# Optimization experiments

Hardware: AMD Instinct MI355X
Metric: run time of the kernel (lower is better)

Reference implementation:

```python
import jax, jax.numpy as jnp
import numpy as np

EPS = 1e-6
BASE_CURVATURE = 1.0


def _artanh(x):
    return jnp.arctanh(jnp.clip(x, -1.0 + 1e-5, 1.0 - 1e-5))


def _norm(x):
    return jnp.maximum(jnp.linalg.norm(x, axis=-1, keepdims=True), EPS)


def _logmap0(x, c):
    # Poincare-ball log map at origin
    sc = jnp.sqrt(c)
    n = _norm(x)
    return _artanh(sc * n) * x / (sc * n)


def _expmap0(v, c):
    # Poincare-ball exp map at origin
    sc = jnp.sqrt(c)
    n = _norm(v)
    return jnp.tanh(sc * n) * v / (sc * n)


def _mobius_add(x, y, c):
    x2 = jnp.sum(x * x, axis=-1, keepdims=True)
    y2 = jnp.sum(y * y, axis=-1, keepdims=True)
    xy = jnp.sum(x * y, axis=-1, keepdims=True)
    num = (1.0 + 2.0 * c * xy + c * y2) * x + (1.0 - c * x2) * y
    den = 1.0 + 2.0 * c * xy + (c * c) * x2 * y2
    return num / jnp.maximum(den, EPS)


def _mobius_scalar_mul(t, x, c):
    sc = jnp.sqrt(c)
    n = _norm(x)
    return jnp.tanh(t * _artanh(sc * n)) * x / (sc * n)


def setup_inputs() -> dict:
    key = jax.random.key(0)
    ks = jax.random.split(key, 8)
    B, D_in, D_out, K = 4096, 2048, 2048, 4
    scale_w = np.sqrt(2.0 / (D_in + D_out)) * 0.1
    return {
        "x": jax.random.normal(ks[0], (B, D_in), jnp.float32) * 0.05,
        "weight": jax.random.normal(ks[1], (D_out, D_in), jnp.float32) * scale_w,
        "bias": jax.random.normal(ks[2], (D_out,), jnp.float32) * 0.01,
        "curv_weight": jax.random.normal(ks[3], (1, D_in), jnp.float32) * 0.1,
        "curv_bias": jnp.zeros((1,), jnp.float32),
        "anchors": jax.random.normal(ks[4], (K, D_out), jnp.float32) * 0.3,
        "t_values": jnp.full((K,), 0.5, jnp.float32),
        "anchor_weights": jnp.full((K,), 1.0 / K, jnp.float32),
    }


def reference(x, weight, bias, curv_weight, curv_bias, anchors, t_values, anchor_weights):
    # 1) dynamic curvature prediction: c_i = base_c * softplus(x . w + b), then mean
    logits = x @ curv_weight[0] + curv_bias[0]                 # [B]
    curvatures = BASE_CURVATURE * jax.nn.softplus(logits)      # [B]
    c = jax.lax.stop_gradient(jnp.mean(curvatures))            # scalar (.item() in torch)

    # 2) fused hyperbolic linear: expmap0(logmap0(x) @ W^T + b)
    u = _logmap0(x, c)                                         # [B, D_in]
    h = u @ weight.T + bias                                    # [B, D_out]
    y = _expmap0(h, c)                                         # [B, D_out]

    # 3) geodesic activation: weighted Mobius geodesic toward each anchor
    xe = y[:, None, :]                                         # [B, 1, D]
    a = anchors[None, :, :]                                    # [1, K, D]
    diff = _mobius_add(-xe, a, c)                              # [B, K, D]
    step = _mobius_scalar_mul(t_values[None, :, None], diff, c)
    g = _mobius_add(xe, step, c)                               # [B, K, D]
    w = jax.nn.softmax(anchor_weights)                         # [K]
    return jnp.einsum("bkd,k->bd", g, w)                       # [B, D_out]
```

## Files before the change

kernel.cpp:

```cpp
#include <hip/hip_runtime.h>
#include <stdint.h>

#define B_ROWS 4096
#define D_IN   2048
#define D_OUT  2048
#define KANCH  4

typedef _Float16 half8  __attribute__((ext_vector_type(8)));
typedef _Float16 half4  __attribute__((ext_vector_type(4)));
typedef float    floatx4 __attribute__((ext_vector_type(4)));
typedef const __attribute__((address_space(1))) uint8_t* gptr_t;
typedef __attribute__((address_space(3))) uint8_t* lptr_t;

__device__ __forceinline__ float frcp(float x)   { return __builtin_amdgcn_rcpf(x); }
__device__ __forceinline__ float ftanh(float x)  { float e = __expf(2.f * x); return (e - 1.f) * frcp(e + 1.f); }
__device__ __forceinline__ float fatanh(float z) { return 0.5f * __logf((1.f + z) * frcp(1.f - z)); }

__global__ __launch_bounds__(256) void k_prep(
    const float* __restrict__ x,
    const float* __restrict__ W,
    const float* __restrict__ cw,
    const float* __restrict__ cb,
    const float* __restrict__ bias,
    const float* __restrict__ anchors,
    _Float16* __restrict__ xh,
    _Float16* __restrict__ Wh,
    float* __restrict__ n2x,
    float* __restrict__ spart,
    float* __restrict__ scal)
{
    int tid = threadIdx.x;
    if (blockIdx.x < 1024) {
        int w = tid >> 6, lane = tid & 63;
        int row = blockIdx.x * 4 + w;
        const floatx4* xr = (const floatx4*)(x + (size_t)row * D_IN);
        const floatx4* wr = (const floatx4*)cw;
        _Float16* xo = xh + (size_t)row * D_IN;
        float dot = 0.f, ss = 0.f;
#pragma unroll
        for (int i = 0; i < 8; ++i) {
            int idx = i * 64 + lane;
            floatx4 xv = xr[idx];
            floatx4 wv = wr[idx];
#pragma unroll
            for (int j = 0; j < 4; ++j) {
                dot += xv[j] * wv[j];
                ss  += xv[j] * xv[j];
            }
            half4 h = {(_Float16)xv[0], (_Float16)xv[1], (_Float16)xv[2], (_Float16)xv[3]};
            *(half4*)(xo + idx * 4) = h;
        }
#pragma unroll
        for (int off = 32; off; off >>= 1) {
            dot += __shfl_down(dot, off);
            ss  += __shfl_down(ss, off);
        }
        __shared__ float spw[4];
        if (lane == 0) {
            n2x[row] = ss;
            float z = dot + cb[0];
            spw[w] = (z > 20.f) ? z : log1pf(expf(z));
        }
        __syncthreads();
        if (tid == 0)
            spart[blockIdx.x] = spw[0] + spw[1] + spw[2] + spw[3];
    } else if (blockIdx.x < 2048) {
        int blk = blockIdx.x - 1024;
        const floatx4* W4 = (const floatx4*)W;
#pragma unroll
        for (int i = 0; i < 4; ++i) {
            int idx = blk * 1024 + i * 256 + tid;
            floatx4 v = W4[idx];
            half4 h = {(_Float16)v[0], (_Float16)v[1], (_Float16)v[2], (_Float16)v[3]};
            *(half4*)(Wh + (size_t)idx * 4) = h;
        }
    } else {
        int w = tid >> 6, lane = tid & 63;
        float bf[8], af[KANCH][8];
        *(floatx4*)(bf)     = *(const floatx4*)(bias + tid * 8);
        *(floatx4*)(bf + 4) = *(const floatx4*)(bias + tid * 8 + 4);
#pragma unroll
        for (int k = 0; k < KANCH; ++k) {
            *(floatx4*)(af[k])     = *(const floatx4*)(anchors + (size_t)k * D_OUT + tid * 8);
            *(floatx4*)(af[k] + 4) = *(const floatx4*)(anchors + (size_t)k * D_OUT + tid * 8 + 4);
        }
        float v[9];
#pragma unroll
        for (int q = 0; q < 9; ++q) v[q] = 0.f;
#pragma unroll
        for (int j = 0; j < 8; ++j) {
            v[0] += bf[j] * bf[j];
#pragma unroll
            for (int k = 0; k < KANCH; ++k) {
                v[1 + k] += bf[j] * af[k][j];
                v[5 + k] += af[k][j] * af[k][j];
            }
        }
#pragma unroll
        for (int off = 32; off; off >>= 1)
#pragma unroll
            for (int q = 0; q < 9; ++q) v[q] += __shfl_down(v[q], off);
        __shared__ float red[4][9];
        if (lane == 0)
#pragma unroll
            for (int q = 0; q < 9; ++q) red[w][q] = v[q];
        __syncthreads();
        if (tid == 0)
#pragma unroll
            for (int q = 0; q < 9; ++q)
                scal[1 + q] = red[0][q] + red[1][q] + red[2][q] + red[3][q];
    }
}

template<int KPB>
__global__ __launch_bounds__(256, 4) void k_gemm(
    const _Float16* __restrict__ A,
    const _Float16* __restrict__ W,
    _Float16* __restrict__ P0,
    _Float16* __restrict__ P1)
{
    __shared__ __align__(16) _Float16 As[128 * 64];
    __shared__ __align__(16) _Float16 Bs[128 * 64];
    int tid = threadIdx.x;
    int lane = tid & 63;
    int w = tid >> 6;
    int wm = (w >> 1) * 64, wn = (w & 1) * 64;
    int bm0 = blockIdx.y * 128, bn0 = blockIdx.x * 128;
    _Float16* P = (blockIdx.z == 0) ? P0 : P1;
    int kbase = blockIdx.z * KPB;

    floatx4 acc[4][4];
#pragma unroll
    for (int mi = 0; mi < 4; ++mi)
#pragma unroll
        for (int ni = 0; ni < 4; ++ni)
            acc[mi][ni] = (floatx4){0.f, 0.f, 0.f, 0.f};

    for (int k0 = 0; k0 < KPB; k0 += 64) {
#pragma unroll
        for (int i = 0; i < 4; ++i) {
            int e = (i * 256 + tid) * 8;
            int r = e >> 6, kk = e & 63;
            __builtin_amdgcn_global_load_lds(
                (gptr_t)(A + (size_t)(bm0 + r) * D_IN + kbase + k0 + kk),
                (lptr_t)(As + e), 16, 0, 0);
            __builtin_amdgcn_global_load_lds(
                (gptr_t)(W + (size_t)(bn0 + r) * D_IN + kbase + k0 + kk),
                (lptr_t)(Bs + e), 16, 0, 0);
        }
        __syncthreads();
#pragma unroll
        for (int ks = 0; ks < 64; ks += 32) {
            int kq = ks + (lane >> 4) * 8;
            half8 afr[4], bfr[4];
#pragma unroll
            for (int mi = 0; mi < 4; ++mi)
                afr[mi] = *(const half8*)(As + (wm + mi * 16 + (lane & 15)) * 64 + kq);
#pragma unroll
            for (int ni = 0; ni < 4; ++ni)
                bfr[ni] = *(const half8*)(Bs + (wn + ni * 16 + (lane & 15)) * 64 + kq);
#pragma unroll
            for (int mi = 0; mi < 4; ++mi)
#pragma unroll
                for (int ni = 0; ni < 4; ++ni)
                    acc[mi][ni] = __builtin_amdgcn_mfma_f32_16x16x32_f16(
                        afr[mi], bfr[ni], acc[mi][ni], 0, 0, 0);
        }
        __syncthreads();
    }
#pragma unroll
    for (int mi = 0; mi < 4; ++mi) {
#pragma unroll
        for (int r = 0; r < 4; ++r) {
            int gm = bm0 + wm + mi * 16 + (lane >> 4) * 4 + r;
#pragma unroll
            for (int ni = 0; ni < 4; ++ni) {
                int gn = bn0 + wn + ni * 16 + (lane & 15);
                P[(size_t)gm * D_OUT + gn] = (_Float16)acc[mi][ni][r];
            }
        }
    }
}

__global__ __launch_bounds__(256) void k_mobius(
    const _Float16* __restrict__ P0,
    const _Float16* __restrict__ P1,
    const float* __restrict__ bias,
    const float* __restrict__ anchors,
    const float* __restrict__ tv,
    const float* __restrict__ aw,
    const float* __restrict__ n2x,
    const float* __restrict__ spart,
    const float* __restrict__ scal,
    int split,
    float* __restrict__ out)
{
    int tid = threadIdx.x, w = tid >> 6, lane = tid & 63;
    size_t rowoff = (size_t)blockIdx.x * D_OUT;
    float pf[8], bf[8];
    {
        half8 p = *(const half8*)(P0 + rowoff + tid * 8);
#pragma unroll
        for (int j = 0; j < 8; ++j) pf[j] = (float)p[j];
    }
    if (split == 2) {
        half8 q = *(const half8*)(P1 + rowoff + tid * 8);
#pragma unroll
        for (int j = 0; j < 8; ++j) pf[j] += (float)q[j];
    }
    *(floatx4*)(bf)     = *(const floatx4*)(bias + tid * 8);
    *(floatx4*)(bf + 4) = *(const floatx4*)(bias + tid * 8 + 4);
    float af[KANCH][8];
#pragma unroll
    for (int k = 0; k < KANCH; ++k) {
        *(floatx4*)(af[k])     = *(const floatx4*)(anchors + (size_t)k * D_OUT + tid * 8);
        *(floatx4*)(af[k] + 4) = *(const floatx4*)(anchors + (size_t)k * D_OUT + tid * 8 + 4);
    }
    float v[7];
#pragma unroll
    for (int q = 0; q < 7; ++q) v[q] = 0.f;
    {
        floatx4 s4 = ((const floatx4*)spart)[tid];
        v[6] = s4[0] + s4[1] + s4[2] + s4[3];
    }
#pragma unroll
    for (int j = 0; j < 8; ++j) {
        v[0] += pf[j] * pf[j];
        v[1] += pf[j] * bf[j];
#pragma unroll
        for (int k = 0; k < KANCH; ++k) v[2 + k] += pf[j] * af[k][j];
    }
#pragma unroll
    for (int off = 32; off; off >>= 1)
#pragma unroll
        for (int q = 0; q < 7; ++q) v[q] += __shfl_down(v[q], off);
    __shared__ float red[4][7];
    __shared__ float cf[2 + KANCH];
    if (lane == 0)
#pragma unroll
        for (int q = 0; q < 7; ++q) red[w][q] = v[q];
    __syncthreads();
    if (w == 0) {
        int k = lane & 3;
        float pp = red[0][0] + red[1][0] + red[2][0] + red[3][0];
        float pb = red[0][1] + red[1][1] + red[2][1] + red[3][1];
        float pa = red[0][2 + k] + red[1][2 + k] + red[2][2 + k] + red[3][2 + k];
        float spsum = red[0][6] + red[1][6] + red[2][6] + red[3][6];
        float bb = scal[1];
        float ba = scal[2 + k];
        float aa = scal[6 + k];
        float c = spsum * (1.0f / (float)B_ROWS);
        float sc = __builtin_amdgcn_sqrtf(c);
        float nx = fmaxf(__builtin_amdgcn_sqrtf(n2x[blockIdx.x]), 1e-6f);
        float ax = sc * nx;
        float zx = fminf(fmaxf(ax, -1.f + 1e-5f), 1.f - 1e-5f);
        float f = fatanh(zx) * frcp(ax);
        float hh = f * f * pp + 2.f * f * pb + bb;
        float ha = f * pa + ba;
        float ek = __expf(aw[k]);
        float se = ek;
        se += __shfl_xor(se, 1);
        se += __shfl_xor(se, 2);
        float wk = ek * frcp(se);
        float nh = fmaxf(__builtin_amdgcn_sqrtf(hh), 1e-6f);
        float snh = sc * nh;
        float gy = ftanh(snh) * frcp(snh);
        float x2 = gy * gy * hh;
        float B1 = 1.f - c * x2;
        float y2 = aa;
        float dy = gy * ha;
        float A1 = 1.f - 2.f * c * dy + c * y2;
        float den1 = fmaxf(1.f - 2.f * c * dy + c * c * x2 * y2, 1e-6f);
        float rd1 = frcp(den1);
        float al = -A1 * rd1, be = B1 * rd1;
        float nd2 = fmaxf(al * al * x2 + 2.f * al * be * dy + be * be * y2, 0.f);
        float nd = fmaxf(__builtin_amdgcn_sqrtf(nd2), 1e-6f);
        float snd = sc * nd;
        float zc = fminf(fmaxf(snd, -1.f + 1e-5f), 1.f - 1e-5f);
        float s = ftanh(tv[k] * fatanh(zc)) * frcp(snd);
        float y2s = s * s * nd2;
        float xys = s * (al * x2 + be * dy);
        float A2 = 1.f + 2.f * c * xys + c * y2s;
        float den2 = fmaxf(1.f + 2.f * c * xys + c * c * x2 * y2s, 1e-6f);
        float rd2 = frcp(den2);
        float Cy  = (A2 + B1 * s * al) * rd2;
        float Cak = (B1 * s * be) * rd2;
        float chk = wk * Cy;
        chk += __shfl_xor(chk, 1);
        chk += __shfl_xor(chk, 2);
        if (lane == 0) {
            float c0 = gy * chk;
            cf[0] = c0 * f;
            cf[1] = c0;
        }
        if (lane < 4) cf[2 + lane] = wk * Cak;
    }
    __syncthreads();
    float cp = cf[0], cb_ = cf[1];
    float o[8];
#pragma unroll
    for (int j = 0; j < 8; ++j) {
        float val = cp * pf[j] + cb_ * bf[j];
#pragma unroll
        for (int k = 0; k < KANCH; ++k) val += cf[2 + k] * af[k][j];
        o[j] = val;
    }
    *(floatx4*)(out + rowoff + tid * 8)     = *(floatx4*)(o);
    *(floatx4*)(out + rowoff + tid * 8 + 4) = *(floatx4*)(o + 4);
}

extern "C" void kernel_launch(void* const* d_in, const int* in_sizes, int n_in,
                              void* d_out, int out_size, void* d_ws, size_t ws_size,
                              hipStream_t stream) {
    const float* x       = (const float*)d_in[0];
    const float* wt      = (const float*)d_in[1];
    const float* bias    = (const float*)d_in[2];
    const float* cw      = (const float*)d_in[3];
    const float* cb      = (const float*)d_in[4];
    const float* anchors = (const float*)d_in[5];
    const float* tv      = (const float*)d_in[6];
    const float* aw      = (const float*)d_in[7];
    float* out = (float*)d_out;

    _Float16* Wh = (_Float16*)d_ws;
    _Float16* xh = Wh + (size_t)D_OUT * D_IN;
    float* n2x   = (float*)(xh + (size_t)B_ROWS * D_IN);
    float* spart = n2x + B_ROWS;
    float* scal  = spart + 1024;
    _Float16* P0 = (_Float16*)(scal + 16);
    _Float16* P1 = P0 + (size_t)B_ROWS * D_OUT;
    size_t need2 = (size_t)((char*)(P1 + (size_t)B_ROWS * D_OUT) - (char*)d_ws);
    int split = (ws_size >= need2) ? 2 : 1;

    k_prep<<<2049, 256, 0, stream>>>(x, wt, cw, cb, bias, anchors, xh, Wh, n2x, spart, scal);
    if (split == 2)
        k_gemm<D_IN / 2><<<dim3(D_OUT / 128, B_ROWS / 128, 2), 256, 0, stream>>>(xh, Wh, P0, P1);
    else
        k_gemm<D_IN><<<dim3(D_OUT / 128, B_ROWS / 128, 1), 256, 0, stream>>>(xh, Wh, P0, P1);
    k_mobius<<<B_ROWS, 256, 0, stream>>>(P0, P1, bias, anchors, tv, aw, n2x, spart, scal, split, out);
}
```

Baseline: 164.3 us.

## Rewrite GEMM as 256x256 tile, 8-wave, double-buffered swizzled LDS pipeline

Replaces the 128x128, 4-wave GEMM that loaded LDS and then synchronised on every k-tile. The new version uses 256x256 block tiles with 8 waves, each wave computing 128x64. It double-buffers LDS in 32-wide k halves, issuing async global-to-LDS loads for future tiles during MFMA phases. LDS addresses get an XOR swizzle to avoid bank conflicts, and s_setprio raises priority around the MFMA bursts. The hand-counted vmcnt waits and barriers make correctness depend on exact load ordering, and the larger tile yields only 256 blocks (with split-K 2), which may under-fill the device.

```diff
diff --git a/kernel.cpp b/kernel.cpp
--- a/kernel.cpp
+++ b/kernel.cpp
@@ -113,69 +113,117 @@
 }
 
 template<int KPB>
-__global__ __launch_bounds__(256, 4) void k_gemm(
+__global__ __launch_bounds__(512, 2) void k_gemm(
     const _Float16* __restrict__ A,
     const _Float16* __restrict__ W,
     _Float16* __restrict__ P0,
     _Float16* __restrict__ P1)
 {
-    __shared__ __align__(16) _Float16 As[128 * 64];
-    __shared__ __align__(16) _Float16 Bs[128 * 64];
-    int tid = threadIdx.x;
-    int lane = tid & 63;
-    int w = tid >> 6;
-    int wm = (w >> 1) * 64, wn = (w & 1) * 64;
-    int bm0 = blockIdx.y * 128, bn0 = blockIdx.x * 128;
+    constexpr int NT = KPB / 64;
+    __shared__ __align__(16) _Float16 lds[2][2][2][8192];
+    const int tid  = threadIdx.x;
+    const int lane = tid & 63;
+    const int w    = tid >> 6;
+    const int wm   = w >> 2;
+    const int wn   = w & 3;
+    const int bm0  = blockIdx.y * 256;
+    const int bn0  = blockIdx.x * 256;
+    const int kbase = blockIdx.z * KPB;
     _Float16* P = (blockIdx.z == 0) ? P0 : P1;
-    int kbase = blockIdx.z * KPB;
-
-    floatx4 acc[4][4];
-#pragma unroll
-    for (int mi = 0; mi < 4; ++mi)
+
+    const int e0 = tid * 16;
+    const int o0 = e0 ^ ((e0 >> 2) & 0x70) ^ ((e0 >> 4) & 0x10);
+    const size_t asrc = (size_t)(bm0 + (o0 >> 6)) * D_IN + ((o0 & 63) >> 1) + kbase;
+    const size_t bsrc = (size_t)(bn0 + (o0 >> 6)) * D_IN + ((o0 & 63) >> 1) + kbase;
+    const int wmoff = wm * 8192;
+    const int wnoff = wn * 4096;
+    const int loff = ((lane & 15) * 64 + (lane >> 4) * 16) ^ ((lane & 7) << 4);
+
+#define STAGE_Q(OP, D, KH, GP, SRC, KB) do { \
+    uint8_t* qb_ = (uint8_t*)&lds[OP][D][KH][0]; \
+    __builtin_amdgcn_global_load_lds((gptr_t)((GP) + (SRC) + (KB)), (lptr_t)(qb_ + e0), 16, 0, 0); \
+    __builtin_amdgcn_global_load_lds((gptr_t)((GP) + (SRC) + (size_t)128 * D_IN + (KB)), (lptr_t)(qb_ + e0 + 8192), 16, 0, 0); \
+} while (0)
+
+    floatx4 acc[8][4];
+#pragma unroll
+    for (int mi = 0; mi < 8; ++mi)
 #pragma unroll
         for (int ni = 0; ni < 4; ++ni)
             acc[mi][ni] = (floatx4){0.f, 0.f, 0.f, 0.f};
 
-    for (int k0 = 0; k0 < KPB; k0 += 64) {
-#pragma unroll
-        for (int i = 0; i < 4; ++i) {
-            int e = (i * 256 + tid) * 8;
-            int r = e >> 6, kk = e & 63;
-            __builtin_amdgcn_global_load_lds(
-                (gptr_t)(A + (size_t)(bm0 + r) * D_IN + kbase + k0 + kk),
-                (lptr_t)(As + e), 16, 0, 0);
-            __builtin_amdgcn_global_load_lds(
-                (gptr_t)(W + (size_t)(bn0 + r) * D_IN + kbase + k0 + kk),
-                (lptr_t)(Bs + e), 16, 0, 0);
-        }
-        __syncthreads();
-#pragma unroll
-        for (int ks = 0; ks < 64; ks += 32) {
-            int kq = ks + (lane >> 4) * 8;
-            half8 afr[4], bfr[4];
-#pragma unroll
-            for (int mi = 0; mi < 4; ++mi)
-                afr[mi] = *(const half8*)(As + (wm + mi * 16 + (lane & 15)) * 64 + kq);
-#pragma unroll
-            for (int ni = 0; ni < 4; ++ni)
-                bfr[ni] = *(const half8*)(Bs + (wn + ni * 16 + (lane & 15)) * 64 + kq);
-#pragma unroll
-            for (int mi = 0; mi < 4; ++mi)
-#pragma unroll
-                for (int ni = 0; ni < 4; ++ni)
-                    acc[mi][ni] = __builtin_amdgcn_mfma_f32_16x16x32_f16(
-                        afr[mi], bfr[ni], acc[mi][ni], 0, 0, 0);
-        }
-        __syncthreads();
-    }
-#pragma unroll
-    for (int mi = 0; mi < 4; ++mi) {
+    STAGE_Q(0, 0, 0, A, asrc, 0);
+    STAGE_Q(0, 0, 1, A, asrc, 32);
+    STAGE_Q(1, 0, 0, W, bsrc, 0);
+    STAGE_Q(1, 0, 1, W, bsrc, 32);
+    STAGE_Q(0, 1, 0, A, asrc, 64);
+    STAGE_Q(1, 1, 0, W, bsrc, 64);
+    STAGE_Q(1, 1, 1, W, bsrc, 96);
+    asm volatile("s_waitcnt vmcnt(6)" ::: "memory");
+    __builtin_amdgcn_s_barrier();
+    __builtin_amdgcn_sched_barrier(0);
+
+    half8 aq[4], bq[4];
+
+#define LOAD_A4(D, KH, MI0) do { _Pragma("unroll") \
+    for (int mi = 0; mi < 4; ++mi) \
+        aq[mi] = *(const half8*)((const uint8_t*)&lds[0][D][KH][0] + wmoff + ((MI0) + mi) * 1024 + loff); \
+} while (0)
+#define LOAD_B4(D, KH) do { _Pragma("unroll") \
+    for (int ni = 0; ni < 4; ++ni) \
+        bq[ni] = *(const half8*)((const uint8_t*)&lds[1][D][KH][0] + wnoff + ni * 1024 + loff); \
+} while (0)
+#define MFMA16(MI0) do { \
+    __builtin_amdgcn_s_barrier(); \
+    asm volatile("s_waitcnt lgkmcnt(0)" ::: "memory"); \
+    __builtin_amdgcn_sched_barrier(0); \
+    __builtin_amdgcn_s_setprio(1); \
+    _Pragma("unroll") for (int mi = 0; mi < 4; ++mi) \
+    _Pragma("unroll") for (int ni = 0; ni < 4; ++ni) \
+        acc[(MI0) + mi][ni] = __builtin_amdgcn_mfma_f32_16x16x32_f16(aq[mi], bq[ni], acc[(MI0) + mi][ni], 0, 0, 0); \
+    __builtin_amdgcn_s_setprio(0); \
+    __builtin_amdgcn_sched_barrier(0); \
+} while (0)
+#define ENDPH() do { __builtin_amdgcn_s_barrier(); __builtin_amdgcn_sched_barrier(0); } while (0)
+
+#define TILE_BODY(T, D) do { \
+    LOAD_A4(D, 0, 0); LOAD_B4(D, 0); \
+    if ((T) + 1 < NT) STAGE_Q(0, (D) ^ 1, 1, A, asrc, ((T) + 1) * 64 + 32); \
+    MFMA16(0); ENDPH(); \
+    LOAD_A4(D, 0, 4); \
+    if ((T) + 2 < NT) STAGE_Q(1, D, 0, W, bsrc, ((T) + 2) * 64); \
+    MFMA16(4); ENDPH(); \
+    LOAD_A4(D, 1, 0); LOAD_B4(D, 1); \
+    if ((T) + 2 < NT) STAGE_Q(0, D, 0, A, asrc, ((T) + 2) * 64); \
+    MFMA16(0); ENDPH(); \
+    LOAD_A4(D, 1, 4); \
+    if ((T) + 2 < NT) STAGE_Q(1, D, 1, W, bsrc, ((T) + 2) * 64 + 32); \
+    MFMA16(4); \
+    if ((T) < NT - 2) asm volatile("s_waitcnt vmcnt(6)" ::: "memory"); \
+    else              asm volatile("s_waitcnt vmcnt(0)" ::: "memory"); \
+    ENDPH(); \
+} while (0)
+
+    for (int t = 0; t < NT; t += 2) {
+        TILE_BODY(t, 0);
+        TILE_BODY(t + 1, 1);
+    }
+
+#undef TILE_BODY
+#undef ENDPH
+#undef MFMA16
+#undef LOAD_B4
+#undef LOAD_A4
+#undef STAGE_Q
+
+#pragma unroll
+    for (int mi = 0; mi < 8; ++mi) {
 #pragma unroll
         for (int r = 0; r < 4; ++r) {
-            int gm = bm0 + wm + mi * 16 + (lane >> 4) * 4 + r;
+            int gm = bm0 + wm * 128 + mi * 16 + (lane >> 4) * 4 + r;
 #pragma unroll
             for (int ni = 0; ni < 4; ++ni) {
-                int gn = bn0 + wn + ni * 16 + (lane & 15);
+                int gn = bn0 + wn * 64 + ni * 16 + (lane & 15);
                 P[(size_t)gm * D_OUT + gn] = (_Float16)acc[mi][ni][r];
             }
         }
@@ -334,8 +382,8 @@
 
     k_prep<<<2049, 256, 0, stream>>>(x, wt, cw, cb, bias, anchors, xh, Wh, n2x, spart, scal);
     if (split == 2)
-        k_gemm<D_IN / 2><<<dim3(D_OUT / 128, B_ROWS / 128, 2), 256, 0, stream>>>(xh, Wh, P0, P1);
+        k_gemm<D_IN / 2><<<dim3(D_OUT / 256, B_ROWS / 256, 2), 512, 0, stream>>>(xh, Wh, P0, P1);
     else
-        k_gemm<D_IN><<<dim3(D_OUT / 128, B_ROWS / 128, 1), 256, 0, stream>>>(xh, Wh, P0, P1);
+        k_gemm<D_IN><<<dim3(D_OUT / 256, B_ROWS / 256, 1), 512, 0, stream>>>(xh, Wh, P0, P1);
     k_mobius<<<B_ROWS, 256, 0, stream>>>(P0, P1, bias, anchors, tv, aw, n2x, spart, scal, split, out);
 }
```

After: 159.8 us. 2.7% less time.

## Rewrite GEMM with triple-buffered LDS pipeline, 256x128 tiles, and drop split-K

Applied to the files above, without the earlier changes.

Replaces the split-K 128x128 GEMM with a single-pass kernel that uses 256x128 tiles and 8 waves per block. It adds a three-stage LDS buffer with half-tile staging, register double-buffered fragments, explicit vmcnt waits and raised wave priority around MFMAs. Block IDs are swizzled so neighbouring blocks share data in L2. Dropping split-K removes the second partial-product buffer and its readback in the epilogue, at the cost of fewer blocks (256) and heavier hand scheduling.

```diff
diff --git a/kernel.cpp b/kernel.cpp
--- a/kernel.cpp
+++ b/kernel.cpp
@@ -112,22 +112,62 @@
     }
 }
 
-template<int KPB>
-__global__ __launch_bounds__(256, 4) void k_gemm(
+__global__ __launch_bounds__(512, 2) void k_gemm(
     const _Float16* __restrict__ A,
     const _Float16* __restrict__ W,
-    _Float16* __restrict__ P0,
-    _Float16* __restrict__ P1)
+    _Float16* __restrict__ P)
 {
-    __shared__ __align__(16) _Float16 As[128 * 64];
-    __shared__ __align__(16) _Float16 Bs[128 * 64];
-    int tid = threadIdx.x;
-    int lane = tid & 63;
-    int w = tid >> 6;
-    int wm = (w >> 1) * 64, wn = (w & 1) * 64;
-    int bm0 = blockIdx.y * 128, bn0 = blockIdx.x * 128;
-    _Float16* P = (blockIdx.z == 0) ? P0 : P1;
-    int kbase = blockIdx.z * KPB;
+    __shared__ __align__(16) _Float16 lds[3][24576];
+    const int tid  = threadIdx.x;
+    const int lane = tid & 63;
+    const int w    = tid >> 6;
+    const int wm   = w >> 1;
+    const int wn   = w & 1;
+    int bid = blockIdx.y * gridDim.x + blockIdx.x;
+    int swz = (bid & 7) * 32 + (bid >> 3);
+    const int bm0 = (swz >> 4) * 256;
+    const int bn0 = (swz & 15) * 128;
+
+    const int srow  = lane & 15;
+    const int scol8 = (lane >> 4) * 8;
+    const size_t aS = (size_t)(bm0 + w * 16 + srow) * D_IN + scol8;
+    const size_t bS = (size_t)(bn0 + w * 16 + srow) * D_IN + scol8;
+    const int dA0 = w * 1024 + lane * 16;
+    const int dA1 = (8 + w) * 1024 + lane * 16;
+    const int dB  = 32768 + w * 1024 + lane * 16;
+    const int rAbase = wm * 4096 + lane * 16;
+    const int rBbase = 32768 + wn * 4096 + lane * 16;
+
+#define STAGE_H(Q, H, KT) do { \
+    uint8_t* _b = (uint8_t*)&lds[Q][0]; \
+    size_t _k = (size_t)(KT) * 64 + (H) * 32; \
+    __builtin_amdgcn_global_load_lds((gptr_t)(A + aS + _k), (lptr_t)(_b + (H) * 16384 + dA0), 16, 0, 0); \
+    __builtin_amdgcn_global_load_lds((gptr_t)(A + aS + (size_t)128 * D_IN + _k), (lptr_t)(_b + (H) * 16384 + dA1), 16, 0, 0); \
+    __builtin_amdgcn_global_load_lds((gptr_t)(W + bS + _k), (lptr_t)(_b + (H) * 8192 + dB), 16, 0, 0); \
+} while (0)
+
+#define LOADF(AQ, BQ, Q, KH) do { \
+    const uint8_t* _b = (const uint8_t*)&lds[Q][0]; \
+    _Pragma("unroll") for (int i = 0; i < 4; ++i) \
+        AQ[i] = *(const half8*)(_b + (KH) * 16384 + rAbase + i * 1024); \
+    _Pragma("unroll") for (int i = 0; i < 4; ++i) \
+        BQ[i] = *(const half8*)(_b + 32768 - 32768 + (KH) * 8192 + rBbase + i * 1024); \
+} while (0)
+
+#define MFMA16(AQ, BQ) do { \
+    __builtin_amdgcn_s_setprio(1); \
+    _Pragma("unroll") for (int mi = 0; mi < 4; ++mi) \
+    _Pragma("unroll") for (int ni = 0; ni < 4; ++ni) \
+        acc[mi][ni] = __builtin_amdgcn_mfma_f32_16x16x32_f16(AQ[mi], BQ[ni], acc[mi][ni], 0, 0, 0); \
+    __builtin_amdgcn_s_setprio(0); \
+} while (0)
+
+#define PH_SYNC(N) do { \
+    __builtin_amdgcn_sched_barrier(0); \
+    asm volatile("s_waitcnt vmcnt(" #N ")" ::: "memory"); \
+    __builtin_amdgcn_s_barrier(); \
+    __builtin_amdgcn_sched_barrier(0); \
+} while (0)
 
     floatx4 acc[4][4];
 #pragma unroll
@@ -136,46 +176,56 @@
         for (int ni = 0; ni < 4; ++ni)
             acc[mi][ni] = (floatx4){0.f, 0.f, 0.f, 0.f};
 
-    for (int k0 = 0; k0 < KPB; k0 += 64) {
-#pragma unroll
-        for (int i = 0; i < 4; ++i) {
-            int e = (i * 256 + tid) * 8;
-            int r = e >> 6, kk = e & 63;
-            __builtin_amdgcn_global_load_lds(
-                (gptr_t)(A + (size_t)(bm0 + r) * D_IN + kbase + k0 + kk),
-                (lptr_t)(As + e), 16, 0, 0);
-            __builtin_amdgcn_global_load_lds(
-                (gptr_t)(W + (size_t)(bn0 + r) * D_IN + kbase + k0 + kk),
-                (lptr_t)(Bs + e), 16, 0, 0);
-        }
-        __syncthreads();
-#pragma unroll
-        for (int ks = 0; ks < 64; ks += 32) {
-            int kq = ks + (lane >> 4) * 8;
-            half8 afr[4], bfr[4];
-#pragma unroll
-            for (int mi = 0; mi < 4; ++mi)
-                afr[mi] = *(const half8*)(As + (wm + mi * 16 + (lane & 15)) * 64 + kq);
-#pragma unroll
-            for (int ni = 0; ni < 4; ++ni)
-                bfr[ni] = *(const half8*)(Bs + (wn + ni * 16 + (lane & 15)) * 64 + kq);
-#pragma unroll
-            for (int mi = 0; mi < 4; ++mi)
-#pragma unroll
-                for (int ni = 0; ni < 4; ++ni)
-                    acc[mi][ni] = __builtin_amdgcn_mfma_f32_16x16x32_f16(
-                        afr[mi], bfr[ni], acc[mi][ni], 0, 0, 0);
-        }
-        __syncthreads();
-    }
+    STAGE_H(0, 0, 0); STAGE_H(0, 1, 0);
+    STAGE_H(1, 0, 1); STAGE_H(1, 1, 1);
+    asm volatile("s_waitcnt vmcnt(6)" ::: "memory");
+    __builtin_amdgcn_s_barrier();
+    __builtin_amdgcn_sched_barrier(0);
+
+    half8 aqE[4], bqE[4], aqO[4], bqO[4];
+    LOADF(aqE, bqE, 0, 0);
+
+#define TILE_BODY(T, Q0, Q1, Q2) do { \
+    STAGE_H(Q2, 0, (T) + 2); \
+    LOADF(aqO, bqO, Q0, 1); \
+    MFMA16(aqE, bqE); \
+    PH_SYNC(6); \
+    STAGE_H(Q2, 1, (T) + 2); \
+    LOADF(aqE, bqE, Q1, 0); \
+    MFMA16(aqO, bqO); \
+    PH_SYNC(6); \
+} while (0)
+
+    for (int T = 0; T < 30; T += 3) {
+        TILE_BODY(T,     0, 1, 2);
+        TILE_BODY(T + 1, 1, 2, 0);
+        TILE_BODY(T + 2, 2, 0, 1);
+    }
+    LOADF(aqO, bqO, 0, 1);
+    MFMA16(aqE, bqE);
+    PH_SYNC(0);
+    LOADF(aqE, bqE, 1, 0);
+    MFMA16(aqO, bqO);
+    PH_SYNC(0);
+    LOADF(aqO, bqO, 1, 1);
+    MFMA16(aqE, bqE);
+    PH_SYNC(0);
+    MFMA16(aqO, bqO);
+
+#undef TILE_BODY
+#undef PH_SYNC
+#undef MFMA16
+#undef LOADF
+#undef STAGE_H
+
 #pragma unroll
     for (int mi = 0; mi < 4; ++mi) {
 #pragma unroll
         for (int r = 0; r < 4; ++r) {
-            int gm = bm0 + wm + mi * 16 + (lane >> 4) * 4 + r;
+            int gm = bm0 + wm * 64 + mi * 16 + (lane >> 4) * 4 + r;
 #pragma unroll
             for (int ni = 0; ni < 4; ++ni) {
-                int gn = bn0 + wn + ni * 16 + (lane & 15);
+                int gn = bn0 + wn * 64 + ni * 16 + (lane & 15);
                 P[(size_t)gm * D_OUT + gn] = (_Float16)acc[mi][ni][r];
             }
         }
@@ -328,14 +378,8 @@
     float* spart = n2x + B_ROWS;
     float* scal  = spart + 1024;
     _Float16* P0 = (_Float16*)(scal + 16);
-    _Float16* P1 = P0 + (size_t)B_ROWS * D_OUT;
-    size_t need2 = (size_t)((char*)(P1 + (size_t)B_ROWS * D_OUT) - (char*)d_ws);
-    int split = (ws_size >= need2) ? 2 : 1;
 
     k_prep<<<2049, 256, 0, stream>>>(x, wt, cw, cb, bias, anchors, xh, Wh, n2x, spart, scal);
-    if (split == 2)
-        k_gemm<D_IN / 2><<<dim3(D_OUT / 128, B_ROWS / 128, 2), 256, 0, stream>>>(xh, Wh, P0, P1);
-    else
-        k_gemm<D_IN><<<dim3(D_OUT / 128, B_ROWS / 128, 1), 256, 0, stream>>>(xh, Wh, P0, P1);
-    k_mobius<<<B_ROWS, 256, 0, stream>>>(P0, P1, bias, anchors, tv, aw, n2x, spart, scal, split, out);
+    k_gemm<<<dim3(16, 16), 512, 0, stream>>>(xh, Wh, P0);
+    k_mobius<<<B_ROWS, 256, 0, stream>>>(P0, P0, bias, anchors, tv, aw, n2x, spart, scal, 1, out);
 }
```

Result: slower. 169.3 us (+3.1%).

## Restructure GEMM to 256x128 tiles with 512 threads, double-buffered LDS and XCD-aware mapping

Applied to the files above, without the earlier changes.

The fp16 MFMA GEMM moves from 128x128 tiles with 256 threads and a single LDS buffer to 256x128 tiles with 8 waves. K-slices of 32 are double-buffered in LDS, so the next slice's global-to-LDS load is issued before the current slice's MFMAs, leaving one barrier per step. Block indices are remapped so each XCD works on a contiguous group of tiles (and one K-split half), aiming for better L2 reuse. The risks are more LDS per block, which lowers occupancy, and smaller K steps, which mean more barriers overall.

```diff
diff --git a/kernel.cpp b/kernel.cpp
--- a/kernel.cpp
+++ b/kernel.cpp
@@ -113,21 +113,56 @@
 }
 
 template<int KPB>
-__global__ __launch_bounds__(256, 4) void k_gemm(
+__global__ __launch_bounds__(512, 4) void k_gemm(
     const _Float16* __restrict__ A,
     const _Float16* __restrict__ W,
     _Float16* __restrict__ P0,
     _Float16* __restrict__ P1)
 {
-    __shared__ __align__(16) _Float16 As[128 * 64];
-    __shared__ __align__(16) _Float16 Bs[128 * 64];
-    int tid = threadIdx.x;
-    int lane = tid & 63;
-    int w = tid >> 6;
-    int wm = (w >> 1) * 64, wn = (w & 1) * 64;
-    int bm0 = blockIdx.y * 128, bn0 = blockIdx.x * 128;
-    _Float16* P = (blockIdx.z == 0) ? P0 : P1;
-    int kbase = blockIdx.z * KPB;
+    constexpr int NT = KPB / 32;
+    constexpr int NZ = (KPB == D_IN) ? 1 : 2;
+    __shared__ __align__(16) _Float16 lds[2][12288];
+    const int tid  = threadIdx.x;
+    const int lane = tid & 63;
+    const int w    = tid >> 6;
+    const int wm   = w >> 1;
+    const int wn   = w & 1;
+
+    int lin = (blockIdx.z * gridDim.y + blockIdx.y) * gridDim.x + blockIdx.x;
+    int xcd = lin & 7;
+    int i   = lin >> 3;
+    int zz, mt, nt;
+    if (NZ == 2) {
+        zz = xcd & 1;
+        int grp = xcd >> 1;
+        mt = (grp >> 1) * 8 + (i >> 3);
+        nt = (grp & 1) * 8 + (i & 7);
+    } else {
+        zz = 0;
+        mt = (xcd >> 1) * 4 + (i >> 3);
+        nt = (xcd & 1) * 8 + (i & 7);
+    }
+    const int bm0 = mt * 256;
+    const int bn0 = nt * 128;
+    const int kbase = zz * KPB;
+    _Float16* P = (zz == 0) ? P0 : P1;
+
+    const int srow = w * 16 + (lane & 15);
+    const int scol = (lane >> 4) * 8;
+    const size_t asrc = (size_t)(bm0 + srow) * D_IN + scol + kbase;
+    const size_t bsrc = (size_t)(bn0 + srow) * D_IN + scol + kbase;
+    const int eA = tid * 16;
+    const int eB = 16384 + tid * 16;
+    const int rA = wm * 4096 + lane * 16;
+    const int rB = 16384 + wn * 4096 + lane * 16;
+
+#define STAGE_T(Q, T) do { \
+    uint8_t* qb_ = (uint8_t*)&lds[Q][0]; \
+    size_t ko_ = (size_t)(T) * 32; \
+    __builtin_amdgcn_global_load_lds((gptr_t)(A + asrc + ko_), (lptr_t)(qb_ + eA), 16, 0, 0); \
+    __builtin_amdgcn_global_load_lds((gptr_t)(A + asrc + (size_t)128 * D_IN + ko_), (lptr_t)(qb_ + eA + 8192), 16, 0, 0); \
+    __builtin_amdgcn_global_load_lds((gptr_t)(W + bsrc + ko_), (lptr_t)(qb_ + eB), 16, 0, 0); \
+} while (0)
 
     floatx4 acc[4][4];
 #pragma unroll
@@ -136,46 +171,39 @@
         for (int ni = 0; ni < 4; ++ni)
             acc[mi][ni] = (floatx4){0.f, 0.f, 0.f, 0.f};
 
-    for (int k0 = 0; k0 < KPB; k0 += 64) {
-#pragma unroll
-        for (int i = 0; i < 4; ++i) {
-            int e = (i * 256 + tid) * 8;
-            int r = e >> 6, kk = e & 63;
-            __builtin_amdgcn_global_load_lds(
-                (gptr_t)(A + (size_t)(bm0 + r) * D_IN + kbase + k0 + kk),
-                (lptr_t)(As + e), 16, 0, 0);
-            __builtin_amdgcn_global_load_lds(
-                (gptr_t)(W + (size_t)(bn0 + r) * D_IN + kbase + k0 + kk),
-                (lptr_t)(Bs + e), 16, 0, 0);
-        }
-        __syncthreads();
-#pragma unroll
-        for (int ks = 0; ks < 64; ks += 32) {
-            int kq = ks + (lane >> 4) * 8;
-            half8 afr[4], bfr[4];
-#pragma unroll
-            for (int mi = 0; mi < 4; ++mi)
-                afr[mi] = *(const half8*)(As + (wm + mi * 16 + (lane & 15)) * 64 + kq);
-#pragma unroll
-            for (int ni = 0; ni < 4; ++ni)
-                bfr[ni] = *(const half8*)(Bs + (wn + ni * 16 + (lane & 15)) * 64 + kq);
-#pragma unroll
-            for (int mi = 0; mi < 4; ++mi)
-#pragma unroll
-                for (int ni = 0; ni < 4; ++ni)
-                    acc[mi][ni] = __builtin_amdgcn_mfma_f32_16x16x32_f16(
-                        afr[mi], bfr[ni], acc[mi][ni], 0, 0, 0);
-        }
-        __syncthreads();
-    }
+    STAGE_T(0, 0);
+    __syncthreads();
+
+#define TILE_BODY(T, Q) do { \
+    if ((T) + 1 < NT) STAGE_T((Q) ^ 1, (T) + 1); \
+    half8 aq[4], bq[4]; \
+    const uint8_t* qb_ = (const uint8_t*)&lds[Q][0]; \
+    _Pragma("unroll") for (int mi = 0; mi < 4; ++mi) \
+        aq[mi] = *(const half8*)(qb_ + rA + mi * 1024); \
+    _Pragma("unroll") for (int ni = 0; ni < 4; ++ni) \
+        bq[ni] = *(const half8*)(qb_ + rB + ni * 1024); \
+    _Pragma("unroll") for (int mi = 0; mi < 4; ++mi) \
+    _Pragma("unroll") for (int ni = 0; ni < 4; ++ni) \
+        acc[mi][ni] = __builtin_amdgcn_mfma_f32_16x16x32_f16(aq[mi], bq[ni], acc[mi][ni], 0, 0, 0); \
+    __syncthreads(); \
+} while (0)
+
+    for (int t = 0; t < NT; t += 2) {
+        TILE_BODY(t, 0);
+        TILE_BODY(t + 1, 1);
+    }
+
+#undef TILE_BODY
+#undef STAGE_T
+
 #pragma unroll
     for (int mi = 0; mi < 4; ++mi) {
 #pragma unroll
         for (int r = 0; r < 4; ++r) {
-            int gm = bm0 + wm + mi * 16 + (lane >> 4) * 4 + r;
+            int gm = bm0 + wm * 64 + mi * 16 + (lane >> 4) * 4 + r;
 #pragma unroll
             for (int ni = 0; ni < 4; ++ni) {
-                int gn = bn0 + wn + ni * 16 + (lane & 15);
+                int gn = bn0 + wn * 64 + ni * 16 + (lane & 15);
                 P[(size_t)gm * D_OUT + gn] = (_Float16)acc[mi][ni][r];
             }
         }
@@ -334,8 +362,8 @@
 
     k_prep<<<2049, 256, 0, stream>>>(x, wt, cw, cb, bias, anchors, xh, Wh, n2x, spart, scal);
     if (split == 2)
-        k_gemm<D_IN / 2><<<dim3(D_OUT / 128, B_ROWS / 128, 2), 256, 0, stream>>>(xh, Wh, P0, P1);
+        k_gemm<D_IN / 2><<<dim3(16, 16, 2), 512, 0, stream>>>(xh, Wh, P0, P1);
     else
-        k_gemm<D_IN><<<dim3(D_OUT / 128, B_ROWS / 128, 1), 256, 0, stream>>>(xh, Wh, P0, P1);
+        k_gemm<D_IN><<<dim3(16, 16, 1), 512, 0, stream>>>(xh, Wh, P0, P1);
     k_mobius<<<B_ROWS, 256, 0, stream>>>(P0, P1, bias, anchors, tv, aw, n2x, spart, scal, split, out);
 }
```

Result: slower. 171.1 us (+4.2%).
